# Performance work log

Measured on AMD Instinct MI355X. Metric: run time of the kernel, lower is better.

The kernel has to match this reference:

```python
import jax, jax.numpy as jnp
import numpy as np

N = 50000      # nodes
E = 800000     # edges (avg degree 16)
F_IN = 128     # input features
H, C = 4, 16   # heads, per-head out channels -> conv out = 64
D = 128        # target_dim (proj output)
NEG_SLOPE = 0.2
LN_EPS = 1e-5


def setup_inputs() -> dict:
    key = jax.random.key(0)
    ks = jax.random.split(key, 8)
    s_in = 1.0 / np.sqrt(F_IN)
    s_hc = 1.0 / np.sqrt(H * C)
    return {
        "x": jax.random.normal(ks[0], (N, F_IN), jnp.float32),
        "edge_index": jax.random.randint(ks[1], (2, E), 0, N, jnp.int64),
        "W": jax.random.normal(ks[2], (F_IN, H * C), jnp.float32) * s_in,
        "att_src": jax.random.normal(ks[3], (H, C), jnp.float32) * s_hc,
        "att_dst": jax.random.normal(ks[4], (H, C), jnp.float32) * s_hc,
        "bias": jnp.zeros((H * C,), jnp.float32),
        "proj_w": jax.random.normal(ks[5], (D, H * C), jnp.float32) * s_hc,
        "proj_b": jnp.zeros((D,), jnp.float32),
        "gamma": jnp.ones((D,), jnp.float32),
        "beta": jnp.zeros((D,), jnp.float32),
    }


def reference(x, edge_index, W, att_src, att_dst, bias, proj_w, proj_b, gamma, beta):
    src, dst = edge_index[0], edge_index[1]
    # GATConv: per-head linear transform  [N, H, C]
    xp = (x @ W).reshape(N, H, C)
    a_src = jnp.einsum("nhc,hc->nh", xp, att_src)  # [N, H]
    a_dst = jnp.einsum("nhc,hc->nh", xp, att_dst)  # [N, H]
    # raw attention logits per edge, per head  [E, H]
    e = jax.nn.leaky_relu(a_src[src] + a_dst[dst], NEG_SLOPE)
    # segment softmax over incoming edges of each destination node
    m = jax.ops.segment_max(e, dst, num_segments=N)          # [N, H]
    ex = jnp.exp(e - m[dst])                                 # [E, H]
    denom = jax.ops.segment_sum(ex, dst, num_segments=N)     # [N, H]
    alpha = ex / (denom[dst] + 1e-16)                        # [E, H]
    # weighted message aggregation  [N, H, C]
    out = jax.ops.segment_sum(alpha[:, :, None] * xp[src], dst, num_segments=N)
    out = out.reshape(N, H * C) + bias                       # concat heads
    # projection to target_dim
    out = out @ proj_w.T + proj_b                            # [N, D]
    # LayerNorm over feature dim
    mu = out.mean(axis=-1, keepdims=True)
    var = out.var(axis=-1, keepdims=True)
    out = (out - mu) * jax.lax.rsqrt(var + LN_EPS) * gamma + beta
    # activation (relu); dropout=0.0 -> identity
    return jax.nn.relu(out)
```

## Files before the change

kernel.cpp:

```cpp
#include <hip/hip_runtime.h>
#include <hip/hip_bf16.h>


#define LEAKY(x) ((x) > 0.f ? (x) : 0.2f * (x))
#define CHUNK 2048
#define NBUK_PAD 256

typedef __attribute__((ext_vector_type(8))) short bf16x8;
typedef __attribute__((ext_vector_type(4))) float f32x4;

static __device__ __forceinline__ unsigned short f2bf_rne(float f) {
    unsigned u = __float_as_uint(f);
    return (unsigned short)((u + 0x7FFFu + ((u >> 16) & 1u)) >> 16);
}
static __device__ __forceinline__ float bf2f(unsigned short h) {
    return __uint_as_float(((unsigned)h) << 16);
}

__global__ __launch_bounds__(256) void k_prep(
    const float* __restrict__ W, const float* __restrict__ bias,
    const float* __restrict__ proj_w, const float* __restrict__ proj_b,
    unsigned short* __restrict__ Whf, unsigned short* __restrict__ Wlf,
    unsigned short* __restrict__ Phf, unsigned short* __restrict__ Plf,
    float* __restrict__ pb2)
{
    int idx = blockIdx.x * 256 + threadIdx.x;
    if (idx < 8192) {
        int j = idx & 7, lane = (idx >> 3) & 63, ts = idx >> 9;
        int t = ts >> 2, s = ts & 3;
        int k = s * 32 + ((lane >> 4) << 3) + j;
        int n = t * 16 + (lane & 15);
        float w = W[k * 64 + n];
        unsigned short wh = f2bf_rne(w);
        Whf[idx] = wh;
        Wlf[idx] = f2bf_rne(w - bf2f(wh));
    } else if (idx < 16384) {
        int i2 = idx - 8192;
        int j = i2 & 7, lane = (i2 >> 3) & 63, ts = i2 >> 9;
        int t = ts >> 1, s = ts & 1;
        int k = s * 32 + ((lane >> 4) << 3) + j;
        int d = t * 16 + (lane & 15);
        float w = proj_w[d * 64 + k];
        unsigned short wh = f2bf_rne(w);
        Phf[i2] = wh;
        Plf[i2] = f2bf_rne(w - bf2f(wh));
    } else if (idx < 16384 + 128) {
        int d = idx - 16384;
        float s = proj_b[d];
        for (int j = 0; j < 64; j++) s += bias[j] * proj_w[d * 64 + j];
        pb2[d] = s;
    }
}

__global__ __launch_bounds__(256) void k_xw_part1(
    const float* __restrict__ x,
    const unsigned short* __restrict__ Whf, const unsigned short* __restrict__ Wlf,
    const float* __restrict__ att_src, const float* __restrict__ att_dst,
    unsigned short* __restrict__ xp, float* __restrict__ a_src, float* __restrict__ a_dst,
    int n_nodes,
    const int* __restrict__ dst, int* __restrict__ cnt, int E,
    int P, int nbXw)
{
    int bid = blockIdx.x;
    int t = threadIdx.x;
    if (bid % P == P - 1) {
        __shared__ int hist[NBUK_PAD];
        hist[t] = 0;
        __syncthreads();
        int blk = bid / P;
        int e0 = blk * CHUNK;
#pragma unroll
        for (int i = 0; i < CHUNK / 256; i++) {
            int e = e0 + i * 256 + t;
            if (e < E) atomicAdd(&hist[dst[e] >> 8], 1);
        }
        __syncthreads();
        cnt[blk * NBUK_PAD + t] = hist[t];
        return;
    }
    int xb = bid - bid / P;
    if (xb >= nbXw) return;
    int w = t >> 6, lane = t & 63;
    int mbase = xb * 64 + w * 16;
    int mrow = lane & 15, kg = lane >> 4;
    int node = mbase + mrow;
    if (node >= n_nodes) node = n_nodes - 1;

    bf16x8 ah[4], al[4];
#pragma unroll
    for (int s = 0; s < 4; s++) {
        const float* px = x + (size_t)node * 128 + s * 32 + kg * 8;
        float4 v0 = *(const float4*)px;
        float4 v1 = *(const float4*)(px + 4);
        float f[8] = {v0.x, v0.y, v0.z, v0.w, v1.x, v1.y, v1.z, v1.w};
#pragma unroll
        for (int j = 0; j < 8; j++) {
            unsigned short h = f2bf_rne(f[j]);
            ah[s][j] = (short)h;
            al[s][j] = (short)f2bf_rne(f[j] - bf2f(h));
        }
    }

    f32x4 acc[4];
#pragma unroll
    for (int tt = 0; tt < 4; tt++) acc[tt] = (f32x4){0.f, 0.f, 0.f, 0.f};

#pragma unroll
    for (int tt = 0; tt < 4; tt++) {
#pragma unroll
        for (int s = 0; s < 4; s++) {
            size_t fi = (size_t)(((tt * 4 + s) * 64 + lane) * 8);
            bf16x8 bh = *(const bf16x8*)(Whf + fi);
            bf16x8 bl = *(const bf16x8*)(Wlf + fi);
            acc[tt] = __builtin_amdgcn_mfma_f32_16x16x32_bf16(ah[s], bh, acc[tt], 0, 0, 0);
            acc[tt] = __builtin_amdgcn_mfma_f32_16x16x32_bf16(ah[s], bl, acc[tt], 0, 0, 0);
            acc[tt] = __builtin_amdgcn_mfma_f32_16x16x32_bf16(al[s], bh, acc[tt], 0, 0, 0);
        }
    }

#pragma unroll
    for (int tt = 0; tt < 4; tt++) {
        float asv = att_src[tt * 16 + mrow];
        float adv = att_dst[tt * 16 + mrow];
#pragma unroll
        for (int r = 0; r < 4; r++) {
            float v = acc[tt][r];
            int n2 = mbase + kg * 4 + r;
            bool ok = (n2 < n_nodes);
            if (ok) xp[(size_t)n2 * 64 + tt * 16 + mrow] = f2bf_rne(v);
            float ts = v * asv;
            float td = v * adv;
#pragma unroll
            for (int off = 8; off; off >>= 1) {
                ts += __shfl_xor(ts, off);
                td += __shfl_xor(td, off);
            }
            if (mrow == 0 && ok) {
                a_src[n2 * 4 + tt] = ts;
                a_dst[n2 * 4 + tt] = td;
            }
        }
    }
}

__global__ __launch_bounds__(256) void k_scanB1(int* __restrict__ cnt, int* __restrict__ bt,
                                                int nchunk)
{
    __shared__ int sh[256];
    int t = threadIdx.x, b = blockIdx.x;
    int v0 = (t < nchunk) ? cnt[t * NBUK_PAD + b] : 0;
    int v1 = (t + 256 < nchunk) ? cnt[(t + 256) * NBUK_PAD + b] : 0;
    sh[t] = v0; __syncthreads();
    for (int off = 1; off < 256; off <<= 1) {
        int u = (t >= off) ? sh[t - off] : 0;
        __syncthreads();
        sh[t] += u;
        __syncthreads();
    }
    int incl0 = sh[t], tot0 = sh[255];
    __syncthreads();
    sh[t] = v1; __syncthreads();
    for (int off = 1; off < 256; off <<= 1) {
        int u = (t >= off) ? sh[t - off] : 0;
        __syncthreads();
        sh[t] += u;
        __syncthreads();
    }
    int incl1 = sh[t] + tot0;
    if (t < nchunk) cnt[t * NBUK_PAD + b] = incl0 - v0;
    if (t + 256 < nchunk) cnt[(t + 256) * NBUK_PAD + b] = incl1 - v1;
    if (t == 255) bt[b] = incl1;
}

__global__ __launch_bounds__(256) void k_scanB2(const int* __restrict__ bt, int* __restrict__ bb,
                                                int* __restrict__ row_ptr, int n_nodes, int E)
{
    __shared__ int sh[256];
    int t = threadIdx.x;
    int v = bt[t];
    sh[t] = v; __syncthreads();
    for (int off = 1; off < 256; off <<= 1) {
        int u = (t >= off) ? sh[t - off] : 0;
        __syncthreads();
        sh[t] += u;
        __syncthreads();
    }
    bb[t] = sh[t] - v;
    if (t == 255) bb[256] = sh[255];
    if (t == 0) row_ptr[n_nodes] = E;
}

__global__ __launch_bounds__(256) void k_part2(const int* __restrict__ src, const int* __restrict__ dst,
                                               const int* __restrict__ cnt, const int* __restrict__ bb,
                                               unsigned* __restrict__ part, int E)
{
    __shared__ int bases[NBUK_PAD];
    int t = threadIdx.x, blk = blockIdx.x;
    bases[t] = cnt[blk * NBUK_PAD + t] + bb[t];
    __syncthreads();
    int e0 = blk * CHUNK;
#pragma unroll
    for (int i = 0; i < CHUNK / 256; i++) {
        int e = e0 + i * 256 + t;
        if (e < E) {
            int d = dst[e];
            int s = src[e];
            int pos = atomicAdd(&bases[d >> 8], 1);
            part[pos] = ((unsigned)s << 8) | (unsigned)(d & 255);
        }
    }
}

__global__ __launch_bounds__(256) void k_csr(const unsigned* __restrict__ part, const int* __restrict__ bb,
                                             int* __restrict__ row_ptr, int* __restrict__ colsrc,
                                             int n_nodes)
{
    __shared__ int hist[256], off[256], sh[256];
    int t = threadIdx.x, b = blockIdx.x;
    int e0 = bb[b], e1 = bb[b + 1];
    int m = e1 - e0;
    hist[t] = 0;
    __syncthreads();
    for (int i = t; i < m; i += 256)
        atomicAdd(&hist[part[e0 + i] & 255u], 1);
    __syncthreads();
    int v = hist[t];
    sh[t] = v; __syncthreads();
    for (int o = 1; o < 256; o <<= 1) {
        int u = (t >= o) ? sh[t - o] : 0;
        __syncthreads();
        sh[t] += u;
        __syncthreads();
    }
    int excl = sh[t] - v;
    off[t] = excl;
    int node = b * 256 + t;
    if (node < n_nodes) row_ptr[node] = e0 + excl;
    __syncthreads();
    for (int i = t; i < m; i += 256) {
        unsigned u = part[e0 + i];
        int pos = atomicAdd(&off[u & 255u], 1);
        colsrc[e0 + pos] = (int)(u >> 8);
    }
}

__global__ __launch_bounds__(256, 8) void k_agg2(
    const unsigned short* __restrict__ xp, const float* __restrict__ a_src, const float* __restrict__ a_dst,
    const int* __restrict__ row_ptr, const int* __restrict__ colsrc,
    unsigned short* __restrict__ aggr, int n_nodes)
{
    __shared__ int   sstage[4][64];
    __shared__ float alpha_s[4][64][4];
    int t = threadIdx.x, w = t >> 6, lane = t & 63;
    int cgrp = lane & 15;
    int epar = lane >> 4;
    int h = cgrp >> 2;
    int n = blockIdx.x * 4 + w;
    if (n >= n_nodes) return;
    int rp0 = row_ptr[n], rp1 = row_ptr[n + 1];
    float4 ad4 = *(const float4*)&a_dst[(size_t)n * 4];
    float ax = 0.f, ay = 0.f, az = 0.f, aw = 0.f, den = 0.f;
    for (int base = rp0; base < rp1; base += 64) {
        int cnt = rp1 - base; if (cnt > 64) cnt = 64;
        int s = 0;
        float4 p = make_float4(0.f, 0.f, 0.f, 0.f);
        if (lane < cnt) {
            s = colsrc[base + lane];
            float4 as4 = *(const float4*)&a_src[(size_t)s * 4];
            p.x = __expf(LEAKY(as4.x + ad4.x));
            p.y = __expf(LEAKY(as4.y + ad4.y));
            p.z = __expf(LEAKY(as4.z + ad4.z));
            p.w = __expf(LEAKY(as4.w + ad4.w));
        }
        sstage[w][lane] = s;
        *(float4*)&alpha_s[w][lane][0] = p;
        int iters = (cnt + 3) >> 2;
        for (int it = 0; it < iters; ++it) {
            int j = (it << 2) + epar;
            int sj = sstage[w][j];
            float aj = alpha_s[w][j][h];
            ushort4 v = *(const ushort4*)(xp + (size_t)((unsigned)sj * 64u + (cgrp << 2)));
            den += aj;
            ax += aj * bf2f(v.x);
            ay += aj * bf2f(v.y);
            az += aj * bf2f(v.z);
            aw += aj * bf2f(v.w);
        }
    }
    ax += __shfl_xor(ax, 16); ax += __shfl_xor(ax, 32);
    ay += __shfl_xor(ay, 16); ay += __shfl_xor(ay, 32);
    az += __shfl_xor(az, 16); az += __shfl_xor(az, 32);
    aw += __shfl_xor(aw, 16); aw += __shfl_xor(aw, 32);
    den += __shfl_xor(den, 16); den += __shfl_xor(den, 32);
    if (lane < 16) {
        float inv = 1.f / (den + 1e-16f);
        ushort4 o;
        o.x = f2bf_rne(ax * inv);
        o.y = f2bf_rne(ay * inv);
        o.z = f2bf_rne(az * inv);
        o.w = f2bf_rne(aw * inv);
        *(ushort4*)(aggr + (size_t)n * 64 + (cgrp << 2)) = o;
    }
}

__global__ __launch_bounds__(256, 4) void k_proj(
    const unsigned short* __restrict__ aggr,
    const unsigned short* __restrict__ Phf, const unsigned short* __restrict__ Plf,
    const float* __restrict__ pb2, const float* __restrict__ gamma, const float* __restrict__ beta,
    float* __restrict__ out, int n_nodes)
{
    __shared__ float pb_s[128], g_s[128], b_s[128];
    int t = threadIdx.x;
    if (t < 128) { pb_s[t] = pb2[t]; g_s[t] = gamma[t]; b_s[t] = beta[t]; }
    __syncthreads();
    int w = t >> 6, lane = t & 63;
    int mbase = blockIdx.x * 64 + w * 16;
    int mrow = lane & 15, kg = lane >> 4;
    int node = mbase + mrow;
    if (node >= n_nodes) node = n_nodes - 1;

    bf16x8 ah[2];
#pragma unroll
    for (int s = 0; s < 2; s++) {
        ah[s] = *(const bf16x8*)(aggr + (size_t)node * 64 + s * 32 + kg * 8);
    }

    f32x4 acc[8];
#pragma unroll
    for (int tt = 0; tt < 8; tt++) acc[tt] = (f32x4){0.f, 0.f, 0.f, 0.f};
#pragma unroll
    for (int tt = 0; tt < 8; tt++) {
#pragma unroll
        for (int s = 0; s < 2; s++) {
            size_t fi = (size_t)(((tt * 2 + s) * 64 + lane) * 8);
            bf16x8 bh = *(const bf16x8*)(Phf + fi);
            bf16x8 bl = *(const bf16x8*)(Plf + fi);
            acc[tt] = __builtin_amdgcn_mfma_f32_16x16x32_bf16(ah[s], bh, acc[tt], 0, 0, 0);
            acc[tt] = __builtin_amdgcn_mfma_f32_16x16x32_bf16(ah[s], bl, acc[tt], 0, 0, 0);
        }
    }

#pragma unroll
    for (int r = 0; r < 4; r++) {
        int nr = mbase + kg * 4 + r;
        float vv[8];
        float S = 0.f, Q = 0.f;
#pragma unroll
        for (int tt = 0; tt < 8; tt++) {
            float v = acc[tt][r] + pb_s[tt * 16 + mrow];
            vv[tt] = v;
            S += v;
            Q += v * v;
        }
#pragma unroll
        for (int off = 8; off; off >>= 1) {
            S += __shfl_xor(S, off);
            Q += __shfl_xor(Q, off);
        }
        float mu  = S * (1.f / 128.f);
        float var = Q * (1.f / 128.f) - mu * mu;
        float inv = rsqrtf(var + 1e-5f);
        if (nr < n_nodes) {
#pragma unroll
            for (int tt = 0; tt < 8; tt++) {
                int d = tt * 16 + mrow;
                float o = fmaxf((vv[tt] - mu) * inv * g_s[d] + b_s[d], 0.f);
                out[(size_t)nr * 128 + d] = o;
            }
        }
    }
}

extern "C" void kernel_launch(void* const* d_in, const int* in_sizes, int n_in,
                              void* d_out, int out_size, void* d_ws, size_t ws_size,
                              hipStream_t stream)
{
    const float* x       = (const float*)d_in[0];
    const int*   ei      = (const int*)  d_in[1];
    const float* W       = (const float*)d_in[2];
    const float* att_src = (const float*)d_in[3];
    const float* att_dst = (const float*)d_in[4];
    const float* bias    = (const float*)d_in[5];
    const float* proj_w  = (const float*)d_in[6];
    const float* proj_b  = (const float*)d_in[7];
    const float* gamma   = (const float*)d_in[8];
    const float* beta    = (const float*)d_in[9];

    int N = in_sizes[0] / 128;
    int E = in_sizes[1] / 2;
    const int* srcIdx = ei;
    const int* dstIdx = ei + E;

    int nchunk = (E + CHUNK - 1) / CHUNK;
    int NBUK   = (N + 255) / 256;
    int nbXw   = (N + 63) / 64;

    char* ws = (char*)d_ws;
    unsigned short* xp   = (unsigned short*)ws; ws += (size_t)N * 64 * 2;
    unsigned short* aggr = (unsigned short*)ws; ws += (size_t)N * 64 * 2;
    float* a_src   = (float*)ws; ws += (size_t)N * 4 * 4;
    float* a_dst   = (float*)ws; ws += (size_t)N * 4 * 4;
    int*   row_ptr = (int*)ws;   ws += (size_t)(N + 1) * 4;
    int*   cnt     = (int*)ws;   ws += (size_t)nchunk * NBUK_PAD * 4;
    unsigned* part = (unsigned*)ws; ws += (size_t)E * 4;
    int*   colsrc  = (int*)ws;   ws += (size_t)E * 4;
    int*   bb      = (int*)ws;   ws += 257 * 4;
    int*   bt      = (int*)ws;   ws += 256 * 4;
    unsigned short* Whf = (unsigned short*)ws; ws += 8192 * 2;
    unsigned short* Wlf = (unsigned short*)ws; ws += 8192 * 2;
    unsigned short* Phf = (unsigned short*)ws; ws += 8192 * 2;
    unsigned short* Plf = (unsigned short*)ws; ws += 8192 * 2;
    float* pb2 = (float*)ws; ws += 128 * 4;

    int P = (nbXw + nchunk - 1) / nchunk + 1;
    int totalFused = nchunk * P;

    k_prep<<<(16512 + 255) / 256, 256, 0, stream>>>(W, bias, proj_w, proj_b,
                                                    Whf, Wlf, Phf, Plf, pb2);
    k_xw_part1<<<totalFused, 256, 0, stream>>>(x, Whf, Wlf, att_src, att_dst,
                                               xp, a_src, a_dst, N,
                                               dstIdx, cnt, E, P, nbXw);
    k_scanB1<<<256, 256, 0, stream>>>(cnt, bt, nchunk);
    k_scanB2<<<1, 256, 0, stream>>>(bt, bb, row_ptr, N, E);
    k_part2<<<nchunk, 256, 0, stream>>>(srcIdx, dstIdx, cnt, bb, part, E);
    k_csr<<<NBUK, 256, 0, stream>>>(part, bb, row_ptr, colsrc, N);
    k_agg2<<<(N + 3) / 4, 256, 0, stream>>>(xp, a_src, a_dst, row_ptr, colsrc, aggr, N);
    k_proj<<<(N + 63) / 64, 256, 0, stream>>>(aggr, Phf, Plf, pb2, gamma, beta, (float*)d_out, N);
}
```

Before: 88.78 us.

## Regroup kernel fusion and widen aggregation gather to 8 channels

Moves the dst histogram into the weight-prep kernel and fuses the scatter partition pass with the x@W GEMM, so the expensive GEMM runs alongside the partition work rather than alongside the histogram. The GEMM now stages x rows through shared memory with coalesced float4 loads before building the MFMA operands. The aggregation kernel gathers 8 bf16 channels per lane and processes 8 edges per iteration instead of 4, which halves the loop trip count at the cost of more registers and an extra shuffle stage. The larger shared-memory footprint (about 34KB per block) may lower occupancy of the fused kernel.

```diff
diff --git a/kernel.cpp b/kernel.cpp
--- a/kernel.cpp
+++ b/kernel.cpp
@@ -7,6 +7,7 @@
 #define NBUK_PAD 256
 
 typedef __attribute__((ext_vector_type(8))) short bf16x8;
+typedef __attribute__((ext_vector_type(8))) unsigned short u16x8;
 typedef __attribute__((ext_vector_type(4))) float f32x4;
 
 static __device__ __forceinline__ unsigned short f2bf_rne(float f) {
@@ -17,19 +18,35 @@
     return __uint_as_float(((unsigned)h) << 16);
 }
 
-__global__ __launch_bounds__(256) void k_prep(
+__global__ __launch_bounds__(256) void k_prep_part1(
     const float* __restrict__ W, const float* __restrict__ bias,
     const float* __restrict__ proj_w, const float* __restrict__ proj_b,
     unsigned short* __restrict__ Whf, unsigned short* __restrict__ Wlf,
     unsigned short* __restrict__ Phf, unsigned short* __restrict__ Plf,
-    float* __restrict__ pb2)
-{
-    int idx = blockIdx.x * 256 + threadIdx.x;
+    float* __restrict__ pb2,
+    const int* __restrict__ dst, int* __restrict__ cnt, int E, int nchunk)
+{
+    int bid = blockIdx.x, t = threadIdx.x;
+    if (bid < nchunk) {
+        __shared__ int hist[NBUK_PAD];
+        hist[t] = 0;
+        __syncthreads();
+        int e0 = bid * CHUNK;
+#pragma unroll
+        for (int i = 0; i < CHUNK / 256; i++) {
+            int e = e0 + i * 256 + t;
+            if (e < E) atomicAdd(&hist[dst[e] >> 8], 1);
+        }
+        __syncthreads();
+        cnt[bid * NBUK_PAD + t] = hist[t];
+        return;
+    }
+    int idx = (bid - nchunk) * 256 + t;
     if (idx < 8192) {
         int j = idx & 7, lane = (idx >> 3) & 63, ts = idx >> 9;
-        int t = ts >> 2, s = ts & 3;
+        int tt = ts >> 2, s = ts & 3;
         int k = s * 32 + ((lane >> 4) << 3) + j;
-        int n = t * 16 + (lane & 15);
+        int n = tt * 16 + (lane & 15);
         float w = W[k * 64 + n];
         unsigned short wh = f2bf_rne(w);
         Whf[idx] = wh;
@@ -37,9 +54,9 @@
     } else if (idx < 16384) {
         int i2 = idx - 8192;
         int j = i2 & 7, lane = (i2 >> 3) & 63, ts = i2 >> 9;
-        int t = ts >> 1, s = ts & 1;
+        int tt = ts >> 1, s = ts & 1;
         int k = s * 32 + ((lane >> 4) << 3) + j;
-        int d = t * 16 + (lane & 15);
+        int d = tt * 16 + (lane & 15);
         float w = proj_w[d * 64 + k];
         unsigned short wh = f2bf_rne(w);
         Phf[i2] = wh;
@@ -52,46 +69,102 @@
     }
 }
 
-__global__ __launch_bounds__(256) void k_xw_part1(
+__global__ __launch_bounds__(256) void k_scanB1(int* __restrict__ cnt, int* __restrict__ bt,
+                                                int nchunk)
+{
+    __shared__ int sh[256];
+    int t = threadIdx.x, b = blockIdx.x;
+    int v0 = (t < nchunk) ? cnt[t * NBUK_PAD + b] : 0;
+    int v1 = (t + 256 < nchunk) ? cnt[(t + 256) * NBUK_PAD + b] : 0;
+    sh[t] = v0; __syncthreads();
+    for (int off = 1; off < 256; off <<= 1) {
+        int u = (t >= off) ? sh[t - off] : 0;
+        __syncthreads();
+        sh[t] += u;
+        __syncthreads();
+    }
+    int incl0 = sh[t], tot0 = sh[255];
+    __syncthreads();
+    sh[t] = v1; __syncthreads();
+    for (int off = 1; off < 256; off <<= 1) {
+        int u = (t >= off) ? sh[t - off] : 0;
+        __syncthreads();
+        sh[t] += u;
+        __syncthreads();
+    }
+    int incl1 = sh[t] + tot0;
+    if (t < nchunk) cnt[t * NBUK_PAD + b] = incl0 - v0;
+    if (t + 256 < nchunk) cnt[(t + 256) * NBUK_PAD + b] = incl1 - v1;
+    if (t == 255) bt[b] = incl1;
+}
+
+__global__ __launch_bounds__(256) void k_scanB2(const int* __restrict__ bt, int* __restrict__ bb,
+                                                int* __restrict__ row_ptr, int n_nodes, int E)
+{
+    __shared__ int sh[256];
+    int t = threadIdx.x;
+    int v = bt[t];
+    sh[t] = v; __syncthreads();
+    for (int off = 1; off < 256; off <<= 1) {
+        int u = (t >= off) ? sh[t - off] : 0;
+        __syncthreads();
+        sh[t] += u;
+        __syncthreads();
+    }
+    bb[t] = sh[t] - v;
+    if (t == 255) bb[256] = sh[255];
+    if (t == 0) row_ptr[n_nodes] = E;
+}
+
+__global__ __launch_bounds__(256) void k_part2_xw(
+    const int* __restrict__ src, const int* __restrict__ dst,
+    const int* __restrict__ cnt, const int* __restrict__ bb,
+    unsigned* __restrict__ part, int E,
     const float* __restrict__ x,
     const unsigned short* __restrict__ Whf, const unsigned short* __restrict__ Wlf,
     const float* __restrict__ att_src, const float* __restrict__ att_dst,
     unsigned short* __restrict__ xp, float* __restrict__ a_src, float* __restrict__ a_dst,
-    int n_nodes,
-    const int* __restrict__ dst, int* __restrict__ cnt, int E,
-    int P, int nbXw)
-{
-    int bid = blockIdx.x;
-    int t = threadIdx.x;
+    int n_nodes, int P, int nbXw)
+{
+    __shared__ float xs[64][132];
+    __shared__ int bases[NBUK_PAD];
+    int bid = blockIdx.x, t = threadIdx.x;
     if (bid % P == P - 1) {
-        __shared__ int hist[NBUK_PAD];
-        hist[t] = 0;
-        __syncthreads();
         int blk = bid / P;
+        bases[t] = cnt[blk * NBUK_PAD + t] + bb[t];
+        __syncthreads();
         int e0 = blk * CHUNK;
 #pragma unroll
         for (int i = 0; i < CHUNK / 256; i++) {
             int e = e0 + i * 256 + t;
-            if (e < E) atomicAdd(&hist[dst[e] >> 8], 1);
-        }
-        __syncthreads();
-        cnt[blk * NBUK_PAD + t] = hist[t];
+            if (e < E) {
+                int d = dst[e];
+                int s = src[e];
+                int pos = atomicAdd(&bases[d >> 8], 1);
+                part[pos] = ((unsigned)s << 8) | (unsigned)(d & 255);
+            }
+        }
         return;
     }
     int xb = bid - bid / P;
     if (xb >= nbXw) return;
+    int xbase = xb * 64;
+    for (int i = t; i < 64 * 32; i += 256) {
+        int r = i >> 5, c = (i & 31) << 2;
+        int gr = xbase + r; if (gr >= n_nodes) gr = n_nodes - 1;
+        *(float4*)&xs[r][c] = *(const float4*)(x + (size_t)gr * 128 + c);
+    }
+    __syncthreads();
     int w = t >> 6, lane = t & 63;
-    int mbase = xb * 64 + w * 16;
+    int mbase = xbase + w * 16;
     int mrow = lane & 15, kg = lane >> 4;
-    int node = mbase + mrow;
-    if (node >= n_nodes) node = n_nodes - 1;
+    int lrow = w * 16 + mrow;
 
     bf16x8 ah[4], al[4];
 #pragma unroll
     for (int s = 0; s < 4; s++) {
-        const float* px = x + (size_t)node * 128 + s * 32 + kg * 8;
-        float4 v0 = *(const float4*)px;
-        float4 v1 = *(const float4*)(px + 4);
+        float4 v0 = *(const float4*)&xs[lrow][s * 32 + kg * 8];
+        float4 v1 = *(const float4*)&xs[lrow][s * 32 + kg * 8 + 4];
         float f[8] = {v0.x, v0.y, v0.z, v0.w, v1.x, v1.y, v1.z, v1.w};
 #pragma unroll
         for (int j = 0; j < 8; j++) {
@@ -104,7 +177,6 @@
     f32x4 acc[4];
 #pragma unroll
     for (int tt = 0; tt < 4; tt++) acc[tt] = (f32x4){0.f, 0.f, 0.f, 0.f};
-
 #pragma unroll
     for (int tt = 0; tt < 4; tt++) {
 #pragma unroll
@@ -143,74 +215,6 @@
     }
 }
 
-__global__ __launch_bounds__(256) void k_scanB1(int* __restrict__ cnt, int* __restrict__ bt,
-                                                int nchunk)
-{
-    __shared__ int sh[256];
-    int t = threadIdx.x, b = blockIdx.x;
-    int v0 = (t < nchunk) ? cnt[t * NBUK_PAD + b] : 0;
-    int v1 = (t + 256 < nchunk) ? cnt[(t + 256) * NBUK_PAD + b] : 0;
-    sh[t] = v0; __syncthreads();
-    for (int off = 1; off < 256; off <<= 1) {
-        int u = (t >= off) ? sh[t - off] : 0;
-        __syncthreads();
-        sh[t] += u;
-        __syncthreads();
-    }
-    int incl0 = sh[t], tot0 = sh[255];
-    __syncthreads();
-    sh[t] = v1; __syncthreads();
-    for (int off = 1; off < 256; off <<= 1) {
-        int u = (t >= off) ? sh[t - off] : 0;
-        __syncthreads();
-        sh[t] += u;
-        __syncthreads();
-    }
-    int incl1 = sh[t] + tot0;
-    if (t < nchunk) cnt[t * NBUK_PAD + b] = incl0 - v0;
-    if (t + 256 < nchunk) cnt[(t + 256) * NBUK_PAD + b] = incl1 - v1;
-    if (t == 255) bt[b] = incl1;
-}
-
-__global__ __launch_bounds__(256) void k_scanB2(const int* __restrict__ bt, int* __restrict__ bb,
-                                                int* __restrict__ row_ptr, int n_nodes, int E)
-{
-    __shared__ int sh[256];
-    int t = threadIdx.x;
-    int v = bt[t];
-    sh[t] = v; __syncthreads();
-    for (int off = 1; off < 256; off <<= 1) {
-        int u = (t >= off) ? sh[t - off] : 0;
-        __syncthreads();
-        sh[t] += u;
-        __syncthreads();
-    }
-    bb[t] = sh[t] - v;
-    if (t == 255) bb[256] = sh[255];
-    if (t == 0) row_ptr[n_nodes] = E;
-}
-
-__global__ __launch_bounds__(256) void k_part2(const int* __restrict__ src, const int* __restrict__ dst,
-                                               const int* __restrict__ cnt, const int* __restrict__ bb,
-                                               unsigned* __restrict__ part, int E)
-{
-    __shared__ int bases[NBUK_PAD];
-    int t = threadIdx.x, blk = blockIdx.x;
-    bases[t] = cnt[blk * NBUK_PAD + t] + bb[t];
-    __syncthreads();
-    int e0 = blk * CHUNK;
-#pragma unroll
-    for (int i = 0; i < CHUNK / 256; i++) {
-        int e = e0 + i * 256 + t;
-        if (e < E) {
-            int d = dst[e];
-            int s = src[e];
-            int pos = atomicAdd(&bases[d >> 8], 1);
-            part[pos] = ((unsigned)s << 8) | (unsigned)(d & 255);
-        }
-    }
-}
-
 __global__ __launch_bounds__(256) void k_csr(const unsigned* __restrict__ part, const int* __restrict__ bb,
                                              int* __restrict__ row_ptr, int* __restrict__ colsrc,
                                              int n_nodes)
@@ -252,14 +256,15 @@
     __shared__ int   sstage[4][64];
     __shared__ float alpha_s[4][64][4];
     int t = threadIdx.x, w = t >> 6, lane = t & 63;
-    int cgrp = lane & 15;
-    int epar = lane >> 4;
-    int h = cgrp >> 2;
+    int cgrp = lane & 7;
+    int eoct = lane >> 3;
+    int h = cgrp >> 1;
     int n = blockIdx.x * 4 + w;
     if (n >= n_nodes) return;
     int rp0 = row_ptr[n], rp1 = row_ptr[n + 1];
     float4 ad4 = *(const float4*)&a_dst[(size_t)n * 4];
-    float ax = 0.f, ay = 0.f, az = 0.f, aw = 0.f, den = 0.f;
+    float acc[8] = {0.f, 0.f, 0.f, 0.f, 0.f, 0.f, 0.f, 0.f};
+    float den = 0.f;
     for (int base = rp0; base < rp1; base += 64) {
         int cnt = rp1 - base; if (cnt > 64) cnt = 64;
         int s = 0;
@@ -274,32 +279,32 @@
         }
         sstage[w][lane] = s;
         *(float4*)&alpha_s[w][lane][0] = p;
-        int iters = (cnt + 3) >> 2;
+        int iters = (cnt + 7) >> 3;
         for (int it = 0; it < iters; ++it) {
-            int j = (it << 2) + epar;
+            int j = (it << 3) + eoct;
             int sj = sstage[w][j];
             float aj = alpha_s[w][j][h];
-            ushort4 v = *(const ushort4*)(xp + (size_t)((unsigned)sj * 64u + (cgrp << 2)));
+            u16x8 v = *(const u16x8*)(xp + (size_t)((unsigned)sj * 64u + (cgrp << 3)));
             den += aj;
-            ax += aj * bf2f(v.x);
-            ay += aj * bf2f(v.y);
-            az += aj * bf2f(v.z);
-            aw += aj * bf2f(v.w);
-        }
-    }
-    ax += __shfl_xor(ax, 16); ax += __shfl_xor(ax, 32);
-    ay += __shfl_xor(ay, 16); ay += __shfl_xor(ay, 32);
-    az += __shfl_xor(az, 16); az += __shfl_xor(az, 32);
-    aw += __shfl_xor(aw, 16); aw += __shfl_xor(aw, 32);
-    den += __shfl_xor(den, 16); den += __shfl_xor(den, 32);
-    if (lane < 16) {
+#pragma unroll
+            for (int q = 0; q < 8; q++) acc[q] += aj * bf2f(v[q]);
+        }
+    }
+#pragma unroll
+    for (int q = 0; q < 8; q++) {
+        acc[q] += __shfl_xor(acc[q], 8);
+        acc[q] += __shfl_xor(acc[q], 16);
+        acc[q] += __shfl_xor(acc[q], 32);
+    }
+    den += __shfl_xor(den, 8);
+    den += __shfl_xor(den, 16);
+    den += __shfl_xor(den, 32);
+    if (eoct == 0) {
         float inv = 1.f / (den + 1e-16f);
-        ushort4 o;
-        o.x = f2bf_rne(ax * inv);
-        o.y = f2bf_rne(ay * inv);
-        o.z = f2bf_rne(az * inv);
-        o.w = f2bf_rne(aw * inv);
-        *(ushort4*)(aggr + (size_t)n * 64 + (cgrp << 2)) = o;
+        u16x8 o;
+#pragma unroll
+        for (int q = 0; q < 8; q++) o[q] = f2bf_rne(acc[q] * inv);
+        *(u16x8*)(aggr + (size_t)n * 64 + (cgrp << 3)) = o;
     }
 }
 
@@ -394,6 +399,7 @@
     int nchunk = (E + CHUNK - 1) / CHUNK;
     int NBUK   = (N + 255) / 256;
     int nbXw   = (N + 63) / 64;
+    int nbPrep = (16512 + 255) / 256;
 
     char* ws = (char*)d_ws;
     unsigned short* xp   = (unsigned short*)ws; ws += (size_t)N * 64 * 2;
@@ -415,14 +421,14 @@
     int P = (nbXw + nchunk - 1) / nchunk + 1;
     int totalFused = nchunk * P;
 
-    k_prep<<<(16512 + 255) / 256, 256, 0, stream>>>(W, bias, proj_w, proj_b,
-                                                    Whf, Wlf, Phf, Plf, pb2);
-    k_xw_part1<<<totalFused, 256, 0, stream>>>(x, Whf, Wlf, att_src, att_dst,
-                                               xp, a_src, a_dst, N,
-                                               dstIdx, cnt, E, P, nbXw);
+    k_prep_part1<<<nchunk + nbPrep, 256, 0, stream>>>(W, bias, proj_w, proj_b,
+                                                      Whf, Wlf, Phf, Plf, pb2,
+                                                      dstIdx, cnt, E, nchunk);
     k_scanB1<<<256, 256, 0, stream>>>(cnt, bt, nchunk);
     k_scanB2<<<1, 256, 0, stream>>>(bt, bb, row_ptr, N, E);
-    k_part2<<<nchunk, 256, 0, stream>>>(srcIdx, dstIdx, cnt, bb, part, E);
+    k_part2_xw<<<totalFused, 256, 0, stream>>>(srcIdx, dstIdx, cnt, bb, part, E,
+                                               x, Whf, Wlf, att_src, att_dst,
+                                               xp, a_src, a_dst, N, P, nbXw);
     k_csr<<<NBUK, 256, 0, stream>>>(part, bb, row_ptr, colsrc, N);
     k_agg2<<<(N + 3) / 4, 256, 0, stream>>>(xp, a_src, a_dst, row_ptr, colsrc, aggr, N);
     k_proj<<<(N + 63) / 64, 256, 0, stream>>>(aggr, Phf, Plf, pb2, gamma, beta, (float*)d_out, N);
```

New measurement: 85.72 us. 1.04x faster.
